# Optimization experiments

Measured on AMD Instinct MI355X. Metric: run time of the kernel, lower is better.

Reference implementation:

```python
import jax, jax.numpy as jnp
import numpy as np

D_MODEL = 512; D_STATE = 64; D_CONV = 4; EXPAND = 2; HEADDIM = 64
D_INNER = EXPAND * D_MODEL          # 1024
NHEADS = D_INNER // HEADDIM         # 16
D_IN_PROJ = 2 * D_INNER + 2 * D_STATE + NHEADS  # z, xBC, dt
CONV_DIM = D_INNER + 2 * D_STATE
BETA = 0.5
BATCH = 8; SEQLEN = 1024
EPS_LN = 1e-12; EPS_RMS = 1e-5


def layernorm(x, w, b, eps=EPS_LN):
    mu = jnp.mean(x, axis=-1, keepdims=True)
    var = jnp.var(x, axis=-1, keepdims=True)
    return (x - mu) * jax.lax.rsqrt(var + eps) * w + b


def causal_dw_conv(x, w, b):
    # x: (b, l, c); w: (c, d_conv) depthwise; causal left-pad d_conv-1
    xt = jnp.transpose(x, (0, 2, 1))                 # (b, c, l)
    k = w[:, None, :]                                # (c, 1, d_conv)
    y = jax.lax.conv_general_dilated(
        xt, k, window_strides=(1,), padding=[(D_CONV - 1, 0)],
        feature_group_count=CONV_DIM,
        dimension_numbers=('NCH', 'OIH', 'NCH'))
    return jnp.transpose(y, (0, 2, 1)) + b


def ssd(x, dt, A, Bm, Cm, Dp):
    # x: (b,l,h,p)  dt: (b,l,h)  A: (h)  Bm,Cm: (b,l,n)  Dp: (h)
    dA = jnp.exp(dt * A)  # (b,l,h) decay per step

    def step(h, inp):
        dA_t, dt_t, B_t, C_t, x_t = inp
        # h: (b, heads, p, n)
        h = h * dA_t[:, :, None, None] + jnp.einsum('bh,bn,bhp->bhpn', dt_t, B_t, x_t)
        y = jnp.einsum('bhpn,bn->bhp', h, C_t)
        return h, y

    init = jnp.zeros((x.shape[0], NHEADS, HEADDIM, D_STATE), x.dtype)
    xs = (jnp.moveaxis(dA, 1, 0), jnp.moveaxis(dt, 1, 0),
          jnp.moveaxis(Bm, 1, 0), jnp.moveaxis(Cm, 1, 0), jnp.moveaxis(x, 1, 0))
    _, ys = jax.lax.scan(step, init, xs)
    y = jnp.moveaxis(ys, 0, 1)           # (b,l,h,p)
    return y + x * Dp[None, None, :, None]


def mamba2(u, in_proj_w, conv_w, conv_b, dt_bias, A_log, Dp, norm_w, out_proj_w):
    zxbcdt = u @ in_proj_w.T                                   # (b,l,D_IN_PROJ)
    z, xBC, dt = jnp.split(zxbcdt, [D_INNER, D_INNER + CONV_DIM], axis=-1)
    dt = jax.nn.softplus(dt + dt_bias)                          # (b,l,h)
    xBC = jax.nn.silu(causal_dw_conv(xBC, conv_w, conv_b))
    x, Bm, Cm = jnp.split(xBC, [D_INNER, D_INNER + D_STATE], axis=-1)
    x = x.reshape(x.shape[0], x.shape[1], NHEADS, HEADDIM)
    A = -jnp.exp(A_log)
    y = ssd(x, dt, A, Bm, Cm, Dp)
    y = y.reshape(y.shape[0], y.shape[1], D_INNER)
    g = y * jax.nn.silu(z)                                      # gated RMSNorm
    g = g * jax.lax.rsqrt(jnp.mean(g * g, axis=-1, keepdims=True) + EPS_RMS) * norm_w
    return g @ out_proj_w.T


def ffn(x, w1, b1, w2, b2, lnw, lnb):
    h = jax.nn.gelu(x @ w1.T + b1, approximate=False)
    h = h @ w2.T + b2
    return layernorm(h + x, lnw, lnb)


def setup_inputs() -> dict:
    key = jax.random.key(0)
    ks = jax.random.split(key, 12)
    item_emb = jax.random.normal(ks[0], (BATCH, SEQLEN, D_MODEL), jnp.float32)
    item_idx = jnp.zeros((BATCH, SEQLEN), jnp.int32)          # single sequence per row
    flip_index = jnp.arange(SEQLEN - 1, -1, -1, dtype=jnp.int64)
    s = 0.02
    in_proj_w = jax.random.normal(ks[1], (D_IN_PROJ, D_MODEL), jnp.float32) * s
    conv_w = jax.random.uniform(ks[2], (CONV_DIM, D_CONV), jnp.float32, -0.5, 0.5)
    conv_b = jnp.zeros((CONV_DIM,), jnp.float32)
    # dt_bias = inverse softplus of dt ~ U[1e-3, 0.1] in log space (mamba init)
    dt = jnp.exp(jax.random.uniform(ks[3], (NHEADS,), jnp.float32,
                                    np.log(1e-3), np.log(0.1)))
    dt_bias = dt + jnp.log(-jnp.expm1(-dt))
    A_log = jnp.log(jax.random.uniform(ks[4], (NHEADS,), jnp.float32, 1.0, 16.0))
    Dp = jnp.ones((NHEADS,), jnp.float32)
    norm_w = jnp.ones((D_INNER,), jnp.float32)
    out_proj_w = jax.random.normal(ks[5], (D_MODEL, D_INNER), jnp.float32) * s
    ln_w = jnp.ones((D_MODEL,), jnp.float32); ln_b = jnp.zeros((D_MODEL,), jnp.float32)
    ffn_w1 = jax.random.normal(ks[6], (4 * D_MODEL, D_MODEL), jnp.float32) * s
    ffn_b1 = jnp.zeros((4 * D_MODEL,), jnp.float32)
    ffn_w2 = jax.random.normal(ks[7], (D_MODEL, 4 * D_MODEL), jnp.float32) * s
    ffn_b2 = jnp.zeros((D_MODEL,), jnp.float32)
    ffn_ln_w = jnp.ones((D_MODEL,), jnp.float32); ffn_ln_b = jnp.zeros((D_MODEL,), jnp.float32)
    return dict(item_emb=item_emb, item_idx=item_idx, flip_index=flip_index,
                in_proj_w=in_proj_w, conv_w=conv_w, conv_b=conv_b, dt_bias=dt_bias,
                A_log=A_log, Dp=Dp, norm_w=norm_w, out_proj_w=out_proj_w,
                ln_w=ln_w, ln_b=ln_b, ffn_w1=ffn_w1, ffn_b1=ffn_b1,
                ffn_w2=ffn_w2, ffn_b2=ffn_b2, ffn_ln_w=ffn_ln_w, ffn_ln_b=ffn_ln_b)


def reference(item_emb, item_idx, flip_index, in_proj_w, conv_w, conv_b, dt_bias,
              A_log, Dp, norm_w, out_proj_w, ln_w, ln_b,
              ffn_w1, ffn_b1, ffn_w2, ffn_b2, ffn_ln_w, ffn_ln_b):
    # item_idx (seq_idx) is all-zeros -> no state resets; dropout is eval-mode identity.
    params = (in_proj_w, conv_w, conv_b, dt_bias, A_log, Dp, norm_w, out_proj_w)
    fwd = mamba2(item_emb, *params)
    bwd = mamba2(item_emb[:, flip_index, :], *params)   # shared weights, as in source
    h = fwd + bwd * BETA + item_emb
    h = layernorm(h, ln_w, ln_b)
    return ffn(h, ffn_w1, ffn_b1, ffn_w2, ffn_b2, ffn_ln_w, ffn_ln_b)
```

## Files before the change

kernel.cpp:

```cpp
#include <hip/hip_runtime.h>
#include <math.h>

#define SEQ     1024
#define NBATCH  8
#define NTOK    8192
#define DMODEL  512
#define DINNER  1024
#define NHEADS  16
#define DPROJ   2192
#define DPROJP  2304
#define CONVDIM 1152
#define DFFN    2048

typedef short bf16x8 __attribute__((ext_vector_type(8)));
typedef float f32x4  __attribute__((ext_vector_type(4)));

__device__ inline unsigned short f2bf(float f) {
  union { float f; unsigned int u; } v; v.f = f;
  unsigned int u = v.u;
  return (unsigned short)((u + 0x7FFFu + ((u >> 16) & 1u)) >> 16);
}
__device__ inline float bf2f(unsigned short s) {
  union { unsigned int u; float f; } v; v.u = ((unsigned int)s) << 16;
  return v.f;
}

__device__ inline float fexp(float x) { return __expf(x); }
__device__ inline float frcp(float x) { return __builtin_amdgcn_rcpf(x); }
__device__ inline float silu_f(float v) { return v * frcp(1.f + fexp(-v)); }
__device__ inline float gelu_f(float v) {
  float x = v * 0.7071067811865476f;
  float ax = fabsf(x);
  float t = frcp(1.f + 0.3275911f * ax);
  float p = ((((1.061405429f * t - 1.453152027f) * t + 1.421413741f) * t
              - 0.284496736f) * t + 0.254829592f) * t;
  float er = copysignf(1.f - p * fexp(-ax * ax), x);
  return 0.5f * v * (1.f + er);
}

#define GLDS16(g, l)                                                         \
  __builtin_amdgcn_global_load_lds(                                          \
      (const __attribute__((address_space(1))) unsigned int*)(g),            \
      (__attribute__((address_space(3))) unsigned int*)(l), 16, 0, 0)

__global__ __launch_bounds__(256)
void cvt_all(const float* __restrict__ u, const float* __restrict__ inw,
             const float* __restrict__ outw, const float* __restrict__ w1,
             const float* __restrict__ w2,
             unsigned short* __restrict__ u_bf, unsigned short* __restrict__ winb,
             unsigned short* __restrict__ woutb, unsigned short* __restrict__ w1b,
             unsigned short* __restrict__ w2b) {
  int i = blockIdx.x * 256 + threadIdx.x;
  const int nu = NTOK * DMODEL;
  const int n0 = DPROJP * DMODEL;
  const int n1 = DMODEL * DINNER;
  const int n2 = DFFN * DMODEL;
  const int n3 = DMODEL * DFFN;
  if (i < nu) {
    u_bf[i] = f2bf(u[i]);
  } else if ((i -= nu) < n0) {
    int r = i / DMODEL;
    winb[i] = (r < DPROJ) ? f2bf(inw[i]) : (unsigned short)0;
  } else if ((i -= n0) < n1) {
    woutb[i] = f2bf(outw[i]);
  } else if ((i -= n1) < n2) {
    w1b[i] = f2bf(w1[i]);
  } else if ((i -= n2) < n3) {
    w2b[i] = f2bf(w2[i]);
  }
}

template <int MODE>
__global__ __launch_bounds__(256)
void gemm_bt(const unsigned short* __restrict__ A, const unsigned short* __restrict__ B,
             void* __restrict__ Cout, const float* __restrict__ bias,
             float* __restrict__ aux, int Ksub, int lda, int Nreal, size_t zstrideC) {
  __shared__ unsigned short sA[2][128 * 32];
  __shared__ unsigned short sB[2][128 * 32];
  const int tid = threadIdx.x;
  const int bx = blockIdx.x, by = blockIdx.y, bz = blockIdx.z;
  const int lane = tid & 63;
  const int wave = tid >> 6;
  const int wm = wave >> 1, wn = wave & 1;
  const int arow = tid >> 2;
  const int acol = (tid & 3) << 3;

  const unsigned short* pA = A + (size_t)(by * 128 + arow) * lda + bz * Ksub + acol;
  const unsigned short* pB = B + (size_t)(bx * 128 + arow) * lda + bz * Ksub + acol;
  const size_t stride64 = (size_t)64 * lda;
  char* sAw[2] = { (char*)&sA[0][0] + wave * 1024, (char*)&sA[1][0] + wave * 1024 };
  char* sBw[2] = { (char*)&sB[0][0] + wave * 1024, (char*)&sB[1][0] + wave * 1024 };

  f32x4 acc[4][4];
#pragma unroll
  for (int i = 0; i < 4; i++)
#pragma unroll
    for (int j = 0; j < 4; j++) { f32x4 z = {0.f, 0.f, 0.f, 0.f}; acc[i][j] = z; }

  GLDS16(pA, sAw[0]);
  GLDS16(pA + stride64, sAw[0] + 4096);
  GLDS16(pB, sBw[0]);
  GLDS16(pB + stride64, sBw[0] + 4096);
  pA += 32; pB += 32;
  __syncthreads();

  const int lrow = lane & 15;
  const int lkq = (lane >> 4) << 3;
  int cur = 0;
  for (int k0 = 0; k0 < Ksub; k0 += 32) {
    if (k0 + 32 < Ksub) {
      const int nxt = cur ^ 1;
      GLDS16(pA, sAw[nxt]);
      GLDS16(pA + stride64, sAw[nxt] + 4096);
      GLDS16(pB, sBw[nxt]);
      GLDS16(pB + stride64, sBw[nxt] + 4096);
      pA += 32; pB += 32;
    }
    bf16x8 af[4], bfr[4];
#pragma unroll
    for (int mi = 0; mi < 4; mi++)
      af[mi] = *(const bf16x8*)&sA[cur][(wm * 64 + mi * 16 + lrow) * 32 + lkq];
#pragma unroll
    for (int ni = 0; ni < 4; ni++)
      bfr[ni] = *(const bf16x8*)&sB[cur][(wn * 64 + ni * 16 + lrow) * 32 + lkq];
#pragma unroll
    for (int mi = 0; mi < 4; mi++)
#pragma unroll
      for (int ni = 0; ni < 4; ni++)
        acc[mi][ni] = __builtin_amdgcn_mfma_f32_16x16x32_bf16(af[mi], bfr[ni], acc[mi][ni], 0, 0, 0);
    __syncthreads();
    cur ^= 1;
  }

  const int row0 = by * 128 + wm * 64;
  const int col0 = bx * 128 + wn * 64;
  float* outf = (float*)Cout;
  unsigned short* outp16 = (unsigned short*)Cout + (size_t)bz * zstrideC;
#pragma unroll
  for (int mi = 0; mi < 4; mi++) {
#pragma unroll
    for (int ni = 0; ni < 4; ni++) {
      const int col = col0 + ni * 16 + lrow;
      if (col < Nreal) {
        const float bval = (MODE == 0 || MODE == 1) && bias ? bias[col] : 0.f;
#pragma unroll
        for (int r = 0; r < 4; r++) {
          const int row = row0 + mi * 16 + ((lane >> 4) << 2) + r;
          float v = acc[mi][ni][r] + bval;
          if (MODE == 1) {
            ((unsigned short*)Cout)[(size_t)row * Nreal + col] = f2bf(gelu_f(v));
          } else if (MODE == 2) {
            ((unsigned short*)Cout)[(size_t)row * Nreal + col] = f2bf(v);
            if (col >= 2176) aux[(size_t)row * 16 + (col - 2176)] = v;
          } else if (MODE == 3) {
            outp16[(size_t)row * Nreal + col] = f2bf(v);
          } else {
            outf[(size_t)row * Nreal + col] = v;
          }
        }
      }
    }
  }
}

__global__ __launch_bounds__(256)
void dt_conv_bc(const float* __restrict__ zdt, const float* __restrict__ dt_bias,
                float* __restrict__ dtf, float* __restrict__ dtb,
                const unsigned short* __restrict__ zxb, const float* __restrict__ cw,
                const float* __restrict__ cb,
                unsigned short* __restrict__ xbcf, unsigned short* __restrict__ xbcb) {
  const int tid = threadIdx.x;
  if (blockIdx.x < 1024) {
    int i = blockIdx.x * 256 + tid;
    int dir = i >> 17;
    int rem = i & 131071;
    int row = rem >> 10;
    int t = rem & 1023;
    int b = row >> 4, h = row & 15;
    int srow = (b << 10) + (dir ? (1023 - t) : t);
    float v = zdt[(size_t)srow * 16 + h] + dt_bias[h];
    float dt = (v > 20.f) ? v : log1pf(fexp(v));
    (dir ? dtb : dtf)[(row << 10) + t] = dt;
    return;
  }
  const int bid = blockIdx.x - 1024;
  const int sx = bid & 15, b = bid >> 4;
  const int c128 = tid & 127;
  const int c = 1024 + c128;
  const int seg = sx * 2 + (tid >> 7);
  const int t0 = seg << 5;
  const float w0 = cw[c * 4 + 0], w1 = cw[c * 4 + 1], w2 = cw[c * 4 + 2], w3 = cw[c * 4 + 3];
  const float bias = cb[c];
  const unsigned short* src = zxb + (size_t)(b << 10) * DPROJ + DINNER + c;
  unsigned short* dstf = xbcf + (size_t)(b << 10) * 128 + c128;
  unsigned short* dstb = xbcb + (size_t)(b << 10) * 128 + c128;
  float r0 = 0.f, r1 = 0.f, r2 = 0.f;
  if (t0 >= 3) {
    r0 = bf2f(src[(size_t)(t0 - 3) * DPROJ]);
    r1 = bf2f(src[(size_t)(t0 - 2) * DPROJ]);
    r2 = bf2f(src[(size_t)(t0 - 1) * DPROJ]);
  }
  for (int s = t0; s < t0 + 32; s++) {
    float x = bf2f(src[(size_t)s * DPROJ]);
    float vf = bias + w0 * r0 + w1 * r1 + w2 * r2 + w3 * x;
    dstf[(size_t)s * 128] = f2bf(silu_f(vf));
    int tp = 1026 - s;
    if (tp <= 1023) {
      float vb = bias + w0 * x + w1 * r2 + w2 * r1 + w3 * r0;
      dstb[(size_t)tp * 128] = f2bf(silu_f(vb));
    }
    r0 = r1; r1 = r2; r2 = x;
  }
  if (seg == 31) {
    float v2 = bias + w1 * r2 + w2 * r1 + w3 * r0;
    float v1 = bias + w2 * r2 + w3 * r1;
    float v0 = bias + w3 * r2;
    dstb[(size_t)2 * 128] = f2bf(silu_f(v2));
    dstb[(size_t)1 * 128] = f2bf(silu_f(v1));
    dstb[0] = f2bf(silu_f(v0));
  }
}

__global__ __launch_bounds__(512)
void ssd_chunk(const unsigned short* __restrict__ zxb,
               const unsigned short* __restrict__ xbcf, const unsigned short* __restrict__ xbcb,
               const float* __restrict__ cw, const float* __restrict__ cb,
               const float* __restrict__ dtf, const float* __restrict__ dtb,
               const float* __restrict__ A_log, const float* __restrict__ Dp,
               unsigned short* __restrict__ yf, unsigned short* __restrict__ yb) {
  const int blk = blockIdx.x;
  const int dir = blk >> 7;
  const int b = (blk >> 4) & 7;
  const int h = blk & 15;
  const unsigned short* xbc = dir ? xbcb : xbcf;
  const float* dts = (dir ? dtb : dtf) + ((size_t)((b << 4) + h) << 10);
  unsigned short* yo = dir ? yb : yf;
  const float A = -expf(A_log[h]);
  const float Dh = Dp[h];
  const int tid = threadIdx.x;
  const int lane = tid & 63;
  const int w = tid >> 6;
  const int wm = w >> 1;
  const int wn = w & 1;
  const int lrow = lane & 15;
  const int quad = lane >> 4;
  const int lk8 = quad << 3;
  const int bS = b << 10;

  __shared__ unsigned short Cb[2][64 * 72];
  __shared__ unsigned short Bb[2][64 * 72];
  __shared__ unsigned short Xt[2][64 * 72];
  __shared__ unsigned short Bt[2][64 * 72];
  __shared__ unsigned short Hb[2][64 * 72];
  __shared__ unsigned short Mb[64 * 72];
  __shared__ float sdt_all[1024];
  __shared__ float Lv_all[16][64];
  __shared__ float ev_all[16][64];
  __shared__ float wv_all[16][64];
  __shared__ float dtot_all[16];

  const unsigned short* bcrow = xbc + (size_t)(bS + (tid >> 3)) * 128 + (tid & 7) * 8;
  const int pr = tid & 31;
  const int sg = tid >> 5;
  const int ccx = h * 64 + pr * 2;
  const unsigned short* bvrow = xbc + (size_t)(bS + sg * 4) * 128 + pr * 2;
  const float4 wx0 = *(const float4*)(cw + ccx * 4);
  const float4 wx1 = *(const float4*)(cw + (ccx + 1) * 4);
  const float bx0 = cb[ccx], bx1 = cb[ccx + 1];

  uint4 vb, vc;
  unsigned int bv[4];
  unsigned int xin[7];

  auto stage_load = [&](int c) {
    const unsigned short* rp = bcrow + (size_t)c * 64 * 128;
    vb = *(const uint4*)(rp);
    vc = *(const uint4*)(rp + 64);
    const unsigned short* tp = bvrow + (size_t)c * 64 * 128;
#pragma unroll
    for (int k = 0; k < 4; k++) bv[k] = *(const unsigned int*)(tp + (size_t)k * 128);
    const int li0 = c * 64 + sg * 4 - 3;
#pragma unroll
    for (int j = 0; j < 7; j++) {
      const int li = li0 + j;
      const int g = dir ? (1023 - li) : li;
      xin[j] = (g >= 0 && g < 1024)
               ? *(const unsigned int*)(zxb + (size_t)(bS + g) * DPROJ + DINNER + ccx)
               : 0u;
    }
  };

  auto stage_write = [&](int buf, int c) {
    *(uint4*)&Bb[buf][(tid >> 3) * 72 + (tid & 7) * 8] = vb;
    *(uint4*)&Cb[buf][(tid >> 3) * 72 + (tid & 7) * 8] = vc;
    float f0[7], f1[7];
#pragma unroll
    for (int j = 0; j < 7; j++) {
      f0[j] = bf2f((unsigned short)(xin[j] & 0xffff));
      f1[j] = bf2f((unsigned short)(xin[j] >> 16));
    }
    unsigned short x0[4], x1[4], b0[4], b1[4];
#pragma unroll
    for (int k = 0; k < 4; k++) {
      const float ws = wv_all[c][sg * 4 + k];
      float v0 = bx0 + wx0.x * f0[k] + wx0.y * f0[k + 1] + wx0.z * f0[k + 2] + wx0.w * f0[k + 3];
      float v1 = bx1 + wx1.x * f1[k] + wx1.y * f1[k + 1] + wx1.z * f1[k + 2] + wx1.w * f1[k + 3];
      x0[k] = f2bf(silu_f(v0));
      x1[k] = f2bf(silu_f(v1));
      b0[k] = f2bf(bf2f((unsigned short)(bv[k] & 0xffff)) * ws);
      b1[k] = f2bf(bf2f((unsigned short)(bv[k] >> 16)) * ws);
    }
    *(uint2*)&Xt[buf][(pr * 2 + 0) * 72 + sg * 4] = *(const uint2*)x0;
    *(uint2*)&Xt[buf][(pr * 2 + 1) * 72 + sg * 4] = *(const uint2*)x1;
    *(uint2*)&Bt[buf][(pr * 2 + 0) * 72 + sg * 4] = *(const uint2*)b0;
    *(uint2*)&Bt[buf][(pr * 2 + 1) * 72 + sg * 4] = *(const uint2*)b1;
  };

  stage_load(0);

  *(float2*)&sdt_all[tid * 2] = *(const float2*)(dts + tid * 2);
  {
    uint4 z; z.x = 0u; z.y = 0u; z.z = 0u; z.w = 0u;
    *(uint4*)&Hb[0][(tid >> 3) * 72 + (tid & 7) * 8] = z;
  }
  __syncthreads();

#pragma unroll
  for (int r = 0; r < 2; r++) {
    const int c = w * 2 + r;
    float dtl = sdt_all[c * 64 + lane];
    float v = dtl;
#pragma unroll
    for (int off = 1; off < 64; off <<= 1) {
      float o = __shfl_up(v, off);
      if (lane >= off) v += o;
    }
    const float Lv = A * v;
    const float LL = __shfl(Lv, 63);
    Lv_all[c][lane] = Lv;
    ev_all[c][lane] = fexp(Lv);
    wv_all[c][lane] = dtl * fexp(LL - Lv);
    if (lane == 0) dtot_all[c] = fexp(LL);
  }
  __syncthreads();

  stage_write(0, 0);
  stage_load(1);
  __syncthreads();

  f32x4 hacc[2];
#pragma unroll
  for (int j = 0; j < 2; j++) { f32x4 z = {0.f, 0.f, 0.f, 0.f}; hacc[j] = z; }

  int cur = 0;
  for (int c = 0; c < 16; c++) {
    const int t0 = c << 6;

    f32x4 m1[2];
#pragma unroll
    for (int j = 0; j < 2; j++) { f32x4 z = {0.f, 0.f, 0.f, 0.f}; m1[j] = z; }
#pragma unroll
    for (int kq = 0; kq < 2; kq++) {
      bf16x8 af = *(const bf16x8*)&Cb[cur][(wm * 16 + lrow) * 72 + kq * 32 + lk8];
#pragma unroll
      for (int j = 0; j < 2; j++) {
        bf16x8 bf = *(const bf16x8*)&Bb[cur][(wn * 32 + j * 16 + lrow) * 72 + kq * 32 + lk8];
        m1[j] = __builtin_amdgcn_mfma_f32_16x16x32_bf16(af, bf, m1[j], 0, 0, 0);
      }
    }
#pragma unroll
    for (int r = 0; r < 4; r++) {
      const int i = wm * 16 + quad * 4 + r;
      const float Li = Lv_all[c][i];
#pragma unroll
      for (int j = 0; j < 2; j++) {
        const int s = wn * 32 + j * 16 + lrow;
        const float Ls = Lv_all[c][s];
        const float ds = sdt_all[c * 64 + s];
        float val = (s <= i) ? m1[j][r] * fexp(Li - Ls) * ds : 0.f;
        Mb[i * 72 + s] = f2bf(val);
      }
    }
    __syncthreads();

    f32x4 Y[2], T[2], S[2];
#pragma unroll
    for (int j = 0; j < 2; j++) {
      f32x4 z = {0.f, 0.f, 0.f, 0.f};
      Y[j] = z; T[j] = z; S[j] = z;
    }
#pragma unroll
    for (int kq = 0; kq < 2; kq++) {
      bf16x8 am = *(const bf16x8*)&Mb[(wm * 16 + lrow) * 72 + kq * 32 + lk8];
      bf16x8 ac = *(const bf16x8*)&Cb[cur][(wm * 16 + lrow) * 72 + kq * 32 + lk8];
      bf16x8 ax = *(const bf16x8*)&Xt[cur][(wm * 16 + lrow) * 72 + kq * 32 + lk8];
#pragma unroll
      for (int j = 0; j < 2; j++) {
        const int brow = (wn * 32 + j * 16 + lrow) * 72 + kq * 32 + lk8;
        bf16x8 bx = *(const bf16x8*)&Xt[cur][brow];
        bf16x8 bh = *(const bf16x8*)&Hb[cur][brow];
        bf16x8 bw = *(const bf16x8*)&Bt[cur][brow];
        Y[j] = __builtin_amdgcn_mfma_f32_16x16x32_bf16(am, bx, Y[j], 0, 0, 0);
        T[j] = __builtin_amdgcn_mfma_f32_16x16x32_bf16(ac, bh, T[j], 0, 0, 0);
        S[j] = __builtin_amdgcn_mfma_f32_16x16x32_bf16(ax, bw, S[j], 0, 0, 0);
      }
    }

    const float dtot = dtot_all[c];
#pragma unroll
    for (int r = 0; r < 4; r++) {
      const int i = wm * 16 + quad * 4 + r;
      const float ei = ev_all[c][i];
#pragma unroll
      for (int j = 0; j < 2; j++) {
        const int p = wn * 32 + j * 16 + lrow;
        float yv = Y[j][r] + ei * T[j][r] + Dh * bf2f(Xt[cur][p * 72 + i]);
        yo[(size_t)(bS + t0 + i) * DINNER + h * 64 + p] = f2bf(yv);
      }
    }
#pragma unroll
    for (int j = 0; j < 2; j++)
#pragma unroll
      for (int r = 0; r < 4; r++)
        hacc[j][r] = dtot * hacc[j][r] + S[j][r];

    const int nxt = cur ^ 1;
    if (c + 1 < 16) {
#pragma unroll
      for (int j = 0; j < 2; j++)
#pragma unroll
        for (int r = 0; r < 4; r++)
          Hb[nxt][(wm * 16 + quad * 4 + r) * 72 + wn * 32 + j * 16 + lrow] = f2bf(hacc[j][r]);
      stage_write(nxt, c + 1);
      if (c + 2 < 16) stage_load(c + 2);
    }
    __syncthreads();
    cur = nxt;
  }
}

__device__ inline float2 block_sum2_256(float a, float b) {
#pragma unroll
  for (int o = 32; o >= 1; o >>= 1) { a += __shfl_xor(a, o); b += __shfl_xor(b, o); }
  __shared__ float ra[4], rb[4];
  const int lane = threadIdx.x & 63, w = threadIdx.x >> 6;
  if (lane == 0) { ra[w] = a; rb[w] = b; }
  __syncthreads();
  float2 out;
  out.x = ra[0] + ra[1] + ra[2] + ra[3];
  out.y = rb[0] + rb[1] + rb[2] + rb[3];
  return out;
}

__global__ __launch_bounds__(256)
void gate_rms_comb(const unsigned short* __restrict__ yf, const unsigned short* __restrict__ yb,
                   const unsigned short* __restrict__ zxb, const float* __restrict__ nw,
                   unsigned short* __restrict__ comb) {
  const int bt = blockIdx.x;
  const int b = bt >> 10, t = bt & 1023;
  const int zrowb = (b << 10) + (1023 - t);
  const int tid = threadIdx.x;
  ushort4 yf4 = *(const ushort4*)(yf + (size_t)bt * DINNER + tid * 4);
  ushort4 yb4 = *(const ushort4*)(yb + (size_t)bt * DINNER + tid * 4);
  ushort4 zf4 = *(const ushort4*)(zxb + (size_t)bt * DPROJ + tid * 4);
  ushort4 zb4 = *(const ushort4*)(zxb + (size_t)zrowb * DPROJ + tid * 4);
  float gf[4], gb[4];
  gf[0] = bf2f(yf4.x) * silu_f(bf2f(zf4.x));
  gf[1] = bf2f(yf4.y) * silu_f(bf2f(zf4.y));
  gf[2] = bf2f(yf4.z) * silu_f(bf2f(zf4.z));
  gf[3] = bf2f(yf4.w) * silu_f(bf2f(zf4.w));
  gb[0] = bf2f(yb4.x) * silu_f(bf2f(zb4.x));
  gb[1] = bf2f(yb4.y) * silu_f(bf2f(zb4.y));
  gb[2] = bf2f(yb4.z) * silu_f(bf2f(zb4.z));
  gb[3] = bf2f(yb4.w) * silu_f(bf2f(zb4.w));
  float2 sr = block_sum2_256(gf[0]*gf[0] + gf[1]*gf[1] + gf[2]*gf[2] + gf[3]*gf[3],
                             gb[0]*gb[0] + gb[1]*gb[1] + gb[2]*gb[2] + gb[3]*gb[3]);
  float sf = rsqrtf(sr.x * (1.f / 1024.f) + 1e-5f);
  float sb = 0.5f * rsqrtf(sr.y * (1.f / 1024.f) + 1e-5f);
  float4 wv = *(const float4*)(nw + tid * 4);
  unsigned short* o = comb + (size_t)bt * DINNER + tid * 4;
  o[0] = f2bf((gf[0] * sf + gb[0] * sb) * wv.x);
  o[1] = f2bf((gf[1] * sf + gb[1] * sb) * wv.y);
  o[2] = f2bf((gf[2] * sf + gb[2] * sb) * wv.z);
  o[3] = f2bf((gf[3] * sf + gb[3] * sb) * wv.w);
}

__global__ __launch_bounds__(256)
void combine_ln(const unsigned short* __restrict__ mo, const float* __restrict__ u,
                const float* __restrict__ w, const float* __restrict__ bias,
                float* __restrict__ hln, unsigned short* __restrict__ hbf) {
  const int bt = blockIdx.x;
  const int tid = threadIdx.x;
  const float2 uu = *(const float2*)(u + (size_t)bt * DMODEL + tid * 2);
  float vx = uu.x, vy = uu.y;
#pragma unroll
  for (int z = 0; z < 4; z++) {
    ushort2 p = *(const ushort2*)(mo + (size_t)z * NTOK * DMODEL + (size_t)bt * DMODEL + tid * 2);
    vx += bf2f(p.x);
    vy += bf2f(p.y);
  }
  float2 sr = block_sum2_256(vx + vy, vx * vx + vy * vy);
  float mean = sr.x * (1.f / 512.f);
  float var = sr.y * (1.f / 512.f) - mean * mean;
  float inv = rsqrtf(var + 1e-12f);
  float2 wv = *(const float2*)(w + tid * 2);
  float2 bv = *(const float2*)(bias + tid * 2);
  float ox = (vx - mean) * inv * wv.x + bv.x;
  float oy = (vy - mean) * inv * wv.y + bv.y;
  *(float2*)(hln + (size_t)bt * DMODEL + tid * 2) = make_float2(ox, oy);
  hbf[(size_t)bt * DMODEL + tid * 2] = f2bf(ox);
  hbf[(size_t)bt * DMODEL + tid * 2 + 1] = f2bf(oy);
}

__global__ __launch_bounds__(256)
void final_ln(const unsigned short* __restrict__ f2, const float* __restrict__ b2,
              const float* __restrict__ hln,
              const float* __restrict__ w, const float* __restrict__ bias,
              float* __restrict__ outp) {
  const int bt = blockIdx.x;
  const int tid = threadIdx.x;
  const float2 bb = *(const float2*)(b2 + tid * 2);
  const float2 h = *(const float2*)(hln + (size_t)bt * DMODEL + tid * 2);
  float vx = bb.x + h.x;
  float vy = bb.y + h.y;
#pragma unroll
  for (int z = 0; z < 4; z++) {
    ushort2 p = *(const ushort2*)(f2 + (size_t)z * NTOK * DMODEL + (size_t)bt * DMODEL + tid * 2);
    vx += bf2f(p.x);
    vy += bf2f(p.y);
  }
  float2 sr = block_sum2_256(vx + vy, vx * vx + vy * vy);
  float mean = sr.x * (1.f / 512.f);
  float var = sr.y * (1.f / 512.f) - mean * mean;
  float inv = rsqrtf(var + 1e-12f);
  float2 wv = *(const float2*)(w + tid * 2);
  float2 bv = *(const float2*)(bias + tid * 2);
  *(float2*)(outp + (size_t)bt * DMODEL + tid * 2) =
      make_float2((vx - mean) * inv * wv.x + bv.x, (vy - mean) * inv * wv.y + bv.y);
}

extern "C" void kernel_launch(void* const* d_in, const int* in_sizes, int n_in,
                              void* d_out, int out_size, void* d_ws, size_t ws_size,
                              hipStream_t stream) {
  const float* item_emb   = (const float*)d_in[0];
  const float* in_proj_w  = (const float*)d_in[3];
  const float* conv_w     = (const float*)d_in[4];
  const float* conv_b     = (const float*)d_in[5];
  const float* dt_bias    = (const float*)d_in[6];
  const float* A_log      = (const float*)d_in[7];
  const float* Dp         = (const float*)d_in[8];
  const float* norm_w     = (const float*)d_in[9];
  const float* out_proj_w = (const float*)d_in[10];
  const float* ln_w       = (const float*)d_in[11];
  const float* ln_b       = (const float*)d_in[12];
  const float* w1         = (const float*)d_in[13];
  const float* b1         = (const float*)d_in[14];
  const float* w2         = (const float*)d_in[15];
  const float* b2         = (const float*)d_in[16];
  const float* fln_w      = (const float*)d_in[17];
  const float* fln_b      = (const float*)d_in[18];
  float* outp = (float*)d_out;
  char* ws = (char*)d_ws;

  const size_t o_ubf  = 0;
  const size_t o_win  = 8388608;
  const size_t o_wout = 10747904;
  const size_t o_w1   = 11796480;
  const size_t o_w2   = 13893632;
  const size_t o_dtf  = 15990784;
  const size_t o_dtb  = 16515072;
  const size_t o_zdt  = 17039360;
  const size_t o_zxb  = 17563648;
  const size_t o_xcf  = 53477376;
  const size_t o_xbcf = 72351744;
  const size_t o_xbcb = 74448896;
  const size_t o_yf   = 91226112;
  const size_t o_yb   = 108003328;
  const size_t o_comb = o_xcf;
  const size_t o_mo   = o_zxb;
  const size_t o_hln  = o_yb;
  const size_t o_hbf  = o_ubf;
  const size_t o_h1   = o_xbcf;
  const size_t o_f2   = o_zxb;

  unsigned short* u_bf  = (unsigned short*)(ws + o_ubf);
  unsigned short* winb  = (unsigned short*)(ws + o_win);
  unsigned short* woutb = (unsigned short*)(ws + o_wout);
  unsigned short* w1b   = (unsigned short*)(ws + o_w1);
  unsigned short* w2b   = (unsigned short*)(ws + o_w2);
  float* dtf = (float*)(ws + o_dtf);
  float* dtb = (float*)(ws + o_dtb);
  float* zdt = (float*)(ws + o_zdt);
  unsigned short* zxb  = (unsigned short*)(ws + o_zxb);
  unsigned short* xbcf = (unsigned short*)(ws + o_xbcf);
  unsigned short* xbcb = (unsigned short*)(ws + o_xbcb);
  unsigned short* yf  = (unsigned short*)(ws + o_yf);
  unsigned short* yb  = (unsigned short*)(ws + o_yb);
  unsigned short* comb = (unsigned short*)(ws + o_comb);
  unsigned short* mo  = (unsigned short*)(ws + o_mo);
  float* hln = (float*)(ws + o_hln);
  unsigned short* hbf = (unsigned short*)(ws + o_hbf);
  unsigned short* h1b = (unsigned short*)(ws + o_h1);
  unsigned short* f2  = (unsigned short*)(ws + o_f2);

  {
    int n = NTOK * DMODEL + DPROJP * DMODEL + DMODEL * DINNER + DFFN * DMODEL + DMODEL * DFFN;
    cvt_all<<<(n + 255) / 256, 256, 0, stream>>>(item_emb, in_proj_w, out_proj_w, w1, w2,
                                                 u_bf, winb, woutb, w1b, w2b);
  }

  gemm_bt<2><<<dim3(DPROJP / 128, NTOK / 128), 256, 0, stream>>>(
      u_bf, winb, zxb, nullptr, zdt, DMODEL, DMODEL, DPROJ, 0);

  dt_conv_bc<<<1152, 256, 0, stream>>>(zdt, dt_bias, dtf, dtb,
                                       zxb, conv_w, conv_b, xbcf, xbcb);

  ssd_chunk<<<256, 512, 0, stream>>>(zxb, xbcf, xbcb, conv_w, conv_b,
                                     dtf, dtb, A_log, Dp, yf, yb);

  gate_rms_comb<<<NTOK, 256, 0, stream>>>(yf, yb, zxb, norm_w, comb);

  gemm_bt<3><<<dim3(DMODEL / 128, NTOK / 128, 4), 256, 0, stream>>>(
      comb, woutb, mo, nullptr, nullptr, DINNER / 4, DINNER, DMODEL,
      (size_t)NTOK * DMODEL);

  combine_ln<<<NTOK, 256, 0, stream>>>(mo, item_emb, ln_w, ln_b, hln, hbf);

  gemm_bt<1><<<dim3(DFFN / 128, NTOK / 128), 256, 0, stream>>>(
      hbf, w1b, h1b, b1, nullptr, DMODEL, DMODEL, DFFN, 0);

  gemm_bt<3><<<dim3(DMODEL / 128, NTOK / 128, 4), 256, 0, stream>>>(
      h1b, w2b, f2, nullptr, nullptr, DFFN / 4, DFFN, DMODEL,
      (size_t)NTOK * DMODEL);

  final_ln<<<NTOK, 256, 0, stream>>>(f2, b2, hln, fln_w, fln_b, outp);

  (void)in_sizes; (void)n_in; (void)out_size; (void)ws_size;
}
```

Measured before the change: 344.6 us.

## Split SSD chunk kernel across two blocks per head by output-row halves

Each (direction, batch, head) unit is now handled by two blocks that each compute half of the output rows (i). The chunk state recurrence (S/hacc) is recomputed redundantly in both blocks, with the warp mapping changed so each warp handles 16 p-rows by 32 n-columns of the state. C and B fragments are loaded straight from global memory into registers instead of being staged through shared memory, which drops the Cb/Bb buffers. The intent is to double the grid from 256 to 512 blocks to fill more CUs, at the cost of duplicated state-update work and input loads.

Measured after the change: 356.8 us. 1.04x slower.

```diff
diff --git a/kernel.cpp b/kernel.cpp
--- a/kernel.cpp
+++ b/kernel.cpp
@@ -229,9 +229,11 @@
                const float* __restrict__ A_log, const float* __restrict__ Dp,
                unsigned short* __restrict__ yf, unsigned short* __restrict__ yb) {
   const int blk = blockIdx.x;
-  const int dir = blk >> 7;
-  const int b = (blk >> 4) & 7;
-  const int h = blk & 15;
+  const int ih = blk & 1;
+  const int unit = blk >> 1;
+  const int dir = unit >> 7;
+  const int b = (unit >> 4) & 7;
+  const int h = unit & 15;
   const unsigned short* xbc = dir ? xbcb : xbcf;
   const float* dts = (dir ? dtb : dtf) + ((size_t)((b << 4) + h) << 10);
   unsigned short* yo = dir ? yb : yf;
@@ -240,26 +242,27 @@
   const int tid = threadIdx.x;
   const int lane = tid & 63;
   const int w = tid >> 6;
-  const int wm = w >> 1;
-  const int wn = w & 1;
+  const int iw = w >> 2;
+  const int sw = w & 3;
   const int lrow = lane & 15;
   const int quad = lane >> 4;
   const int lk8 = quad << 3;
   const int bS = b << 10;
-
-  __shared__ unsigned short Cb[2][64 * 72];
-  __shared__ unsigned short Bb[2][64 * 72];
+  const int i0 = ih * 32 + iw * 16;
+  const int il0 = iw * 16;
+  const int s0 = sw * 16;
+  const int p0 = sw * 16;
+  const int n0 = iw * 32;
+
   __shared__ unsigned short Xt[2][64 * 72];
   __shared__ unsigned short Bt[2][64 * 72];
   __shared__ unsigned short Hb[2][64 * 72];
-  __shared__ unsigned short Mb[64 * 72];
+  __shared__ unsigned short Mb[32 * 72];
   __shared__ float sdt_all[1024];
   __shared__ float Lv_all[16][64];
-  __shared__ float ev_all[16][64];
   __shared__ float wv_all[16][64];
   __shared__ float dtot_all[16];
 
-  const unsigned short* bcrow = xbc + (size_t)(bS + (tid >> 3)) * 128 + (tid & 7) * 8;
   const int pr = tid & 31;
   const int sg = tid >> 5;
   const int ccx = h * 64 + pr * 2;
@@ -268,14 +271,19 @@
   const float4 wx1 = *(const float4*)(cw + (ccx + 1) * 4);
   const float bx0 = cb[ccx], bx1 = cb[ccx + 1];
 
-  uint4 vb, vc;
   unsigned int bv[4];
   unsigned int xin[7];
-
+  bf16x8 af[2], bfr[2];
+
+  auto frag_load = [&](int c) {
+    const unsigned short* base = xbc + (size_t)(bS + c * 64) * 128;
+#pragma unroll
+    for (int kq = 0; kq < 2; kq++) {
+      af[kq]  = *(const bf16x8*)(base + (size_t)(i0 + lrow) * 128 + 64 + kq * 32 + lk8);
+      bfr[kq] = *(const bf16x8*)(base + (size_t)(s0 + lrow) * 128 + kq * 32 + lk8);
+    }
+  };
   auto stage_load = [&](int c) {
-    const unsigned short* rp = bcrow + (size_t)c * 64 * 128;
-    vb = *(const uint4*)(rp);
-    vc = *(const uint4*)(rp + 64);
     const unsigned short* tp = bvrow + (size_t)c * 64 * 128;
 #pragma unroll
     for (int k = 0; k < 4; k++) bv[k] = *(const unsigned int*)(tp + (size_t)k * 128);
@@ -289,10 +297,7 @@
                : 0u;
     }
   };
-
   auto stage_write = [&](int buf, int c) {
-    *(uint4*)&Bb[buf][(tid >> 3) * 72 + (tid & 7) * 8] = vb;
-    *(uint4*)&Cb[buf][(tid >> 3) * 72 + (tid & 7) * 8] = vc;
     float f0[7], f1[7];
 #pragma unroll
     for (int j = 0; j < 7; j++) {
@@ -316,6 +321,7 @@
     *(uint2*)&Bt[buf][(pr * 2 + 1) * 72 + sg * 4] = *(const uint2*)b1;
   };
 
+  frag_load(0);
   stage_load(0);
 
   *(float2*)&sdt_all[tid * 2] = *(const float2*)(dts + tid * 2);
@@ -338,7 +344,6 @@
     const float Lv = A * v;
     const float LL = __shfl(Lv, 63);
     Lv_all[c][lane] = Lv;
-    ev_all[c][lane] = fexp(Lv);
     wv_all[c][lane] = dtl * fexp(LL - Lv);
     if (lane == 0) dtot_all[c] = fexp(LL);
   }
@@ -356,67 +361,52 @@
   for (int c = 0; c < 16; c++) {
     const int t0 = c << 6;
 
-    f32x4 m1[2];
-#pragma unroll
-    for (int j = 0; j < 2; j++) { f32x4 z = {0.f, 0.f, 0.f, 0.f}; m1[j] = z; }
+    f32x4 m1 = {0.f, 0.f, 0.f, 0.f};
+#pragma unroll
+    for (int kq = 0; kq < 2; kq++)
+      m1 = __builtin_amdgcn_mfma_f32_16x16x32_bf16(af[kq], bfr[kq], m1, 0, 0, 0);
+#pragma unroll
+    for (int r = 0; r < 4; r++) {
+      const int i = i0 + quad * 4 + r;
+      const float Li = Lv_all[c][i];
+      const int s = s0 + lrow;
+      const float Ls = Lv_all[c][s];
+      const float ds = sdt_all[c * 64 + s];
+      float val = (s <= i) ? m1[r] * fexp(Li - Ls) * ds : 0.f;
+      Mb[(il0 + quad * 4 + r) * 72 + s] = f2bf(val);
+    }
+    __syncthreads();
+
+    f32x4 Y = {0.f, 0.f, 0.f, 0.f}, T = {0.f, 0.f, 0.f, 0.f};
+    f32x4 S[2];
+#pragma unroll
+    for (int j = 0; j < 2; j++) { f32x4 z = {0.f, 0.f, 0.f, 0.f}; S[j] = z; }
+    bf16x8 am[2], xp[2];
 #pragma unroll
     for (int kq = 0; kq < 2; kq++) {
-      bf16x8 af = *(const bf16x8*)&Cb[cur][(wm * 16 + lrow) * 72 + kq * 32 + lk8];
+      am[kq] = *(const bf16x8*)&Mb[(il0 + lrow) * 72 + kq * 32 + lk8];
+      xp[kq] = *(const bf16x8*)&Xt[cur][(p0 + lrow) * 72 + kq * 32 + lk8];
+    }
+#pragma unroll
+    for (int kq = 0; kq < 2; kq++) {
+      bf16x8 bh = *(const bf16x8*)&Hb[cur][(p0 + lrow) * 72 + kq * 32 + lk8];
+      Y = __builtin_amdgcn_mfma_f32_16x16x32_bf16(am[kq], xp[kq], Y, 0, 0, 0);
+      T = __builtin_amdgcn_mfma_f32_16x16x32_bf16(af[kq], bh, T, 0, 0, 0);
 #pragma unroll
       for (int j = 0; j < 2; j++) {
-        bf16x8 bf = *(const bf16x8*)&Bb[cur][(wn * 32 + j * 16 + lrow) * 72 + kq * 32 + lk8];
-        m1[j] = __builtin_amdgcn_mfma_f32_16x16x32_bf16(af, bf, m1[j], 0, 0, 0);
+        bf16x8 bw = *(const bf16x8*)&Bt[cur][(n0 + j * 16 + lrow) * 72 + kq * 32 + lk8];
+        S[j] = __builtin_amdgcn_mfma_f32_16x16x32_bf16(xp[kq], bw, S[j], 0, 0, 0);
       }
     }
+
+    const float dtot = dtot_all[c];
+    const int p = p0 + lrow;
 #pragma unroll
     for (int r = 0; r < 4; r++) {
-      const int i = wm * 16 + quad * 4 + r;
-      const float Li = Lv_all[c][i];
-#pragma unroll
-      for (int j = 0; j < 2; j++) {
-        const int s = wn * 32 + j * 16 + lrow;
-        const float Ls = Lv_all[c][s];
-        const float ds = sdt_all[c * 64 + s];
-        float val = (s <= i) ? m1[j][r] * fexp(Li - Ls) * ds : 0.f;
-        Mb[i * 72 + s] = f2bf(val);
-      }
-    }
-    __syncthreads();
-
-    f32x4 Y[2], T[2], S[2];
-#pragma unroll
-    for (int j = 0; j < 2; j++) {
-      f32x4 z = {0.f, 0.f, 0.f, 0.f};
-      Y[j] = z; T[j] = z; S[j] = z;
-    }
-#pragma unroll
-    for (int kq = 0; kq < 2; kq++) {
-      bf16x8 am = *(const bf16x8*)&Mb[(wm * 16 + lrow) * 72 + kq * 32 + lk8];
-      bf16x8 ac = *(const bf16x8*)&Cb[cur][(wm * 16 + lrow) * 72 + kq * 32 + lk8];
-      bf16x8 ax = *(const bf16x8*)&Xt[cur][(wm * 16 + lrow) * 72 + kq * 32 + lk8];
-#pragma unroll
-      for (int j = 0; j < 2; j++) {
-        const int brow = (wn * 32 + j * 16 + lrow) * 72 + kq * 32 + lk8;
-        bf16x8 bx = *(const bf16x8*)&Xt[cur][brow];
-        bf16x8 bh = *(const bf16x8*)&Hb[cur][brow];
-        bf16x8 bw = *(const bf16x8*)&Bt[cur][brow];
-        Y[j] = __builtin_amdgcn_mfma_f32_16x16x32_bf16(am, bx, Y[j], 0, 0, 0);
-        T[j] = __builtin_amdgcn_mfma_f32_16x16x32_bf16(ac, bh, T[j], 0, 0, 0);
-        S[j] = __builtin_amdgcn_mfma_f32_16x16x32_bf16(ax, bw, S[j], 0, 0, 0);
-      }
-    }
-
-    const float dtot = dtot_all[c];
-#pragma unroll
-    for (int r = 0; r < 4; r++) {
-      const int i = wm * 16 + quad * 4 + r;
-      const float ei = ev_all[c][i];
-#pragma unroll
-      for (int j = 0; j < 2; j++) {
-        const int p = wn * 32 + j * 16 + lrow;
-        float yv = Y[j][r] + ei * T[j][r] + Dh * bf2f(Xt[cur][p * 72 + i]);
-        yo[(size_t)(bS + t0 + i) * DINNER + h * 64 + p] = f2bf(yv);
-      }
+      const int i = i0 + quad * 4 + r;
+      const float ei = fexp(Lv_all[c][i]);
+      float yv = Y[r] + ei * T[r] + Dh * bf2f(Xt[cur][p * 72 + i]);
+      yo[(size_t)(bS + t0 + i) * DINNER + h * 64 + p] = f2bf(yv);
     }
 #pragma unroll
     for (int j = 0; j < 2; j++)
@@ -430,9 +420,10 @@
       for (int j = 0; j < 2; j++)
 #pragma unroll
         for (int r = 0; r < 4; r++)
-          Hb[nxt][(wm * 16 + quad * 4 + r) * 72 + wn * 32 + j * 16 + lrow] = f2bf(hacc[j][r]);
+          Hb[nxt][(p0 + quad * 4 + r) * 72 + n0 + j * 16 + lrow] = f2bf(hacc[j][r]);
       stage_write(nxt, c + 1);
       if (c + 2 < 16) stage_load(c + 2);
+      frag_load(c + 1);
     }
     __syncthreads();
     cur = nxt;
@@ -615,7 +606,7 @@
   dt_conv_bc<<<1152, 256, 0, stream>>>(zdt, dt_bias, dtf, dtb,
                                        zxb, conv_w, conv_b, xbcf, xbcb);
 
-  ssd_chunk<<<256, 512, 0, stream>>>(zxb, xbcf, xbcb, conv_w, conv_b,
+  ssd_chunk<<<512, 512, 0, stream>>>(zxb, xbcf, xbcb, conv_w, conv_b,
                                      dtf, dtb, A_log, Dp, yf, yb);
 
   gate_rms_comb<<<NTOK, 256, 0, stream>>>(yf, yb, zxb, norm_w, comb);
```
